# Kernel tuning notes

Measured on AMD Instinct MI355X. Metric: run time of the kernel, lower is better.

The kernel has to match this reference:

```python
import jax, jax.numpy as jnp
import numpy as np

EPS = float(np.finfo(np.float32).eps)


def setup_inputs() -> dict:
    key = jax.random.key(0)
    k1, k2, k3 = jax.random.split(key, 3)
    T, D, E = 8192, 2048, 64
    x = jax.random.normal(k1, (T, D), dtype=jnp.float32)
    wg_weight = jax.random.normal(k2, (E, D), dtype=jnp.float32) * 0.02
    u = jax.random.uniform(k3, (T, E), dtype=jnp.float32, minval=1e-6, maxval=1.0 - 1e-6)
    gumbel_noise = -jnp.log(-jnp.log(u))  # standard Gumbel(0,1) rsample
    return {"x": x, "wg_weight": wg_weight, "gumbel_noise": gumbel_noise}


def reference(x, wg_weight, gumbel_noise):
    # logits = wg(input): [T, E]
    logits = x @ wg_weight.T
    T, E = logits.shape
    capacity = 2 * ((T + E - 1) // E)  # training mode: 2 * ceil(T/E)

    gates = jax.nn.softmax(logits, axis=1)

    # top-1 expert
    idx1 = jnp.argmax(gates, axis=1)                       # [T]
    mask1 = jax.nn.one_hot(idx1, E, dtype=jnp.float32)     # [T, E]

    # second expert via gumbel-noised logits, masking out expert 1
    logits_w_noise = logits + gumbel_noise
    logits_except1 = jnp.where(mask1 > 0, -jnp.inf, logits_w_noise)
    idx2 = jnp.argmax(logits_except1, axis=1)
    mask2 = jax.nn.one_hot(idx2, E, dtype=jnp.float32)

    # capacity assignment: position of each token in its expert's queue
    locations1 = jnp.cumsum(mask1, axis=0) - 1.0           # [T, E]
    locations2 = jnp.cumsum(mask2, axis=0) - 1.0 + jnp.sum(mask1, axis=0, keepdims=True)

    # aux load-balancing loss
    me = jnp.mean(gates, axis=0)
    ce = jnp.mean(mask1, axis=0)
    l_aux = jnp.mean(me * ce) * E * E

    # drop tokens over capacity
    mask1 = mask1 * (locations1 < capacity)
    mask2 = mask2 * (locations2 < capacity)

    # gate values, renormalized over the two (kept) experts
    gates1_s = jnp.sum(gates * mask1, axis=1)
    gates2_s = jnp.sum(gates * mask2, axis=1)
    denom = jnp.maximum(gates1_s + gates2_s, EPS)
    gates1_s = gates1_s / denom
    gates2_s = gates2_s / denom

    # capacity slot index per token (0 for dropped tokens)
    loc1_s = jnp.sum(locations1 * mask1, axis=1).astype(jnp.int32)   # [T]
    loc2_s = jnp.sum(locations2 * mask2, axis=1).astype(jnp.int32)
    loc1_sc = jax.nn.one_hot(loc1_s, capacity, dtype=jnp.float32)    # [T, C]
    loc2_sc = jax.nn.one_hot(loc2_s, capacity, dtype=jnp.float32)

    # combine_weights[t, e, c] = gate_s[t] * mask[t, e] * onehot_loc[t, c]
    combine1 = jnp.einsum('t,te,tc->tec', gates1_s, mask1, loc1_sc)
    combine2 = jnp.einsum('t,te,tc->tec', gates2_s, mask2, loc2_sc)
    combine_weights = combine1 + combine2                   # [T, E, C]
    dispatch_mask = combine_weights.astype(bool)

    return l_aux, combine_weights, dispatch_mask
```

## Files before the change

kernel.cpp:

```cpp
#include <hip/hip_runtime.h>
#include <math.h>

#define T_TOK 8192
#define D_DIM 2048
#define E_EXP 64
#define CAP   256
#define NCHUNK 32
#define TEC   (134217728LL)
#define TE    (T_TOK * E_EXP)
#define KSPLIT 4
#define KLEN   (D_DIM / KSPLIT)

__device__ __forceinline__ int swz(int r) { return (r & 7) ^ ((r >> 3) & 7); }

__global__ __launch_bounds__(256) void k_gemm(const float* __restrict__ x,
                                              const float* __restrict__ wg,
                                              float* __restrict__ part) {
  __shared__ float xs[64 * 64];
  __shared__ float ws[64 * 64];
  const int tid = threadIdx.x;
  const int row0 = (blockIdx.x >> 2) * 64;
  const int kc = blockIdx.x & 3;
  const int kbase = kc * KLEN;
  const int tr = tid & 15;
  const int tc = tid >> 4;
  const int sA[4] = {swz(tr), swz(tr + 16), swz(tr + 32), swz(tr + 48)};
  const int sB[4] = {swz(tc * 4 + 0), swz(tc * 4 + 1), swz(tc * 4 + 2), swz(tc * 4 + 3)};
  float acc[4][4] = {{0.f, 0.f, 0.f, 0.f}, {0.f, 0.f, 0.f, 0.f},
                     {0.f, 0.f, 0.f, 0.f}, {0.f, 0.f, 0.f, 0.f}};
  for (int k0 = kbase; k0 < kbase + KLEN; k0 += 64) {
#pragma unroll
    for (int i = 0; i < 4; ++i) {
      const int f = tid + i * 256;
      const int r = f >> 4, g = f & 15;
      const float4 v = *reinterpret_cast<const float4*>(
          &x[(size_t)(row0 + r) * D_DIM + k0 + g * 4]);
      *reinterpret_cast<float4*>(&xs[r * 64 + ((g ^ swz(r)) << 2)]) = v;
    }
#pragma unroll
    for (int i = 0; i < 4; ++i) {
      const int f = tid + i * 256;
      const int r = f >> 4, g = f & 15;
      const float4 v = *reinterpret_cast<const float4*>(
          &wg[(size_t)r * D_DIM + k0 + g * 4]);
      *reinterpret_cast<float4*>(&ws[r * 64 + ((g ^ swz(r)) << 2)]) = v;
    }
    __syncthreads();
#pragma unroll
    for (int g = 0; g < 16; ++g) {
      float4 a[4], b[4];
#pragma unroll
      for (int j = 0; j < 4; ++j) {
        a[j] = *reinterpret_cast<const float4*>(&xs[(tr + 16 * j) * 64 + ((g ^ sA[j]) << 2)]);
        b[j] = *reinterpret_cast<const float4*>(&ws[(tc * 4 + j) * 64 + ((g ^ sB[j]) << 2)]);
      }
#pragma unroll
      for (int jr = 0; jr < 4; ++jr)
#pragma unroll
        for (int jc = 0; jc < 4; ++jc) {
          acc[jr][jc] = fmaf(a[jr].x, b[jc].x, acc[jr][jc]);
          acc[jr][jc] = fmaf(a[jr].y, b[jc].y, acc[jr][jc]);
          acc[jr][jc] = fmaf(a[jr].z, b[jc].z, acc[jr][jc]);
          acc[jr][jc] = fmaf(a[jr].w, b[jc].w, acc[jr][jc]);
        }
    }
    __syncthreads();
  }
  float* pbase = part + (size_t)kc * TE;
#pragma unroll
  for (int jr = 0; jr < 4; ++jr) {
    const float4 o = make_float4(acc[jr][0], acc[jr][1], acc[jr][2], acc[jr][3]);
    *reinterpret_cast<float4*>(&pbase[(size_t)(row0 + tr + 16 * jr) * E_EXP + tc * 4]) = o;
  }
}

__global__ __launch_bounds__(256) void k_gate(const float* __restrict__ part,
                                              const float* __restrict__ gumbel,
                                              float* __restrict__ colpart,
                                              int* __restrict__ idx1,
                                              int* __restrict__ idx2,
                                              float* __restrict__ g1v,
                                              float* __restrict__ g2v) {
  const int lane = threadIdx.x & 63;
  const int wave = threadIdx.x >> 6;
  const int gwave = blockIdx.x * 4 + wave;
  float colacc = 0.f;
  for (int i = 0; i < 4; ++i) {
    const int tA = gwave + i * 1024;
    const int tB = tA + 4096;
    const int oA = tA * 64 + lane;
    const int oB = tB * 64 + lane;
    const float LA = (part[oA] + part[TE + oA]) + (part[2 * TE + oA] + part[3 * TE + oA]);
    const float LB = (part[oB] + part[TE + oB]) + (part[2 * TE + oB] + part[3 * TE + oB]);
    const float gnA = gumbel[oA];
    const float gnB = gumbel[oB];
    float mA = LA; int iA = lane;
    float mB = LB; int iB = lane;
#pragma unroll
    for (int off = 32; off; off >>= 1) {
      const float vA = __shfl_xor(mA, off); const int jA = __shfl_xor(iA, off);
      const float vB = __shfl_xor(mB, off); const int jB = __shfl_xor(iB, off);
      if (vA > mA || (vA == mA && jA < iA)) { mA = vA; iA = jA; }
      if (vB > mB || (vB == mB && jB < iB)) { mB = vB; iB = jB; }
    }
    const float eA = expf(LA - mA);
    const float eB = expf(LB - mB);
    float sA = eA, sB = eB;
#pragma unroll
    for (int off = 32; off; off >>= 1) {
      sA += __shfl_xor(sA, off);
      sB += __shfl_xor(sB, off);
    }
    colacc += eA / sA + eB / sB;
    const float gate1A = 1.0f / sA;
    const float gate1B = 1.0f / sB;
    float nA = LA + gnA; if (lane == iA) nA = -INFINITY;
    float nB = LB + gnB; if (lane == iB) nB = -INFINITY;
    float vA2 = nA; int iA2 = lane;
    float vB2 = nB; int iB2 = lane;
#pragma unroll
    for (int off = 32; off; off >>= 1) {
      const float wA = __shfl_xor(vA2, off); const int kA = __shfl_xor(iA2, off);
      const float wB = __shfl_xor(vB2, off); const int kB = __shfl_xor(iB2, off);
      if (wA > vA2 || (wA == vA2 && kA < iA2)) { vA2 = wA; iA2 = kA; }
      if (wB > vB2 || (wB == vB2 && kB < iB2)) { vB2 = wB; iB2 = kB; }
    }
    const float gate2A = __shfl(eA, iA2) / sA;
    const float gate2B = __shfl(eB, iB2) / sB;
    if (lane == 0) {
      idx1[tA] = iA; idx2[tA] = iA2; g1v[tA] = gate1A; g2v[tA] = gate2A;
      idx1[tB] = iB; idx2[tB] = iB2; g1v[tB] = gate1B; g2v[tB] = gate2B;
    }
  }
  __shared__ float cs[4][64];
  cs[wave][lane] = colacc;
  __syncthreads();
  if (wave == 0) {
    float ssum = cs[0][lane] + cs[1][lane] + cs[2][lane] + cs[3][lane];
    colpart[blockIdx.x * 64 + lane] = ssum;
  }
}

__global__ __launch_bounds__(256) void k_rank(const int* __restrict__ idx1,
                                              const int* __restrict__ idx2,
                                              int* __restrict__ rank1,
                                              int* __restrict__ rank2,
                                              int* __restrict__ hist1,
                                              int* __restrict__ hist2) {
  __shared__ int s1[256], s2[256];
  __shared__ int h1[64], h2[64];
  const int tid = threadIdx.x;
  const int base = blockIdx.x * 256;
  if (tid < 64) { h1[tid] = 0; h2[tid] = 0; }
  s1[tid] = idx1[base + tid];
  s2[tid] = idx2[base + tid];
  __syncthreads();
  const int my1 = s1[tid], my2 = s2[tid];
  int r1 = 0, r2 = 0;
  for (int j = 0; j < 256; ++j) {
    r1 += (j < tid && s1[j] == my1);
    r2 += (j < tid && s2[j] == my2);
  }
  atomicAdd(&h1[my1], 1);
  atomicAdd(&h2[my2], 1);
  rank1[base + tid] = r1;
  rank2[base + tid] = r2;
  __syncthreads();
  if (tid < 64) {
    hist1[blockIdx.x * 64 + tid] = h1[tid];
    hist2[blockIdx.x * 64 + tid] = h2[tid];
  }
}

__global__ __launch_bounds__(256) void k_scatter(const int* __restrict__ idx1,
                                                 const int* __restrict__ idx2,
                                                 const float* __restrict__ g1v,
                                                 const float* __restrict__ g2v,
                                                 const int* __restrict__ rank1,
                                                 const int* __restrict__ rank2,
                                                 const int* __restrict__ hist1,
                                                 const int* __restrict__ hist2,
                                                 const float* __restrict__ colpart,
                                                 float* __restrict__ dout) {
  __shared__ int offs1_s[64], offs2_s[64];
  const int tid = threadIdx.x;
  const int bid = blockIdx.x;
  if (tid < 64) {
    const int e = tid;
    int run1 = 0, pre1 = 0;
    for (int c = 0; c < NCHUNK; ++c) {
      if (c == bid) pre1 = run1;
      run1 += hist1[c * 64 + e];
    }
    const int total1 = run1;
    int pre2 = 0;
    for (int c = 0; c < bid; ++c) pre2 += hist2[c * 64 + e];
    offs1_s[e] = pre1;
    offs2_s[e] = total1 + pre2;
    if (bid == 0) {
      float csum = 0.f;
      for (int b = 0; b < 256; ++b) csum += colpart[b * 64 + e];
      const float me = csum / (float)T_TOK;
      const float ce = (float)total1 / (float)T_TOK;
      float val = me * ce;
#pragma unroll
      for (int o = 32; o; o >>= 1) val += __shfl_xor(val, o);
      if (e == 0) dout[0] = val * (float)E_EXP;
    }
  }
  __syncthreads();
  const int t = bid * 256 + tid;
  const int e1 = idx1[t], e2 = idx2[t];
  const int loc1 = offs1_s[e1] + rank1[t];
  const int loc2 = offs2_s[e2] + rank2[t];
  const bool k1 = loc1 < CAP;
  const bool k2 = loc2 < CAP;
  const float a = k1 ? g1v[t] : 0.f;
  const float b = k2 ? g2v[t] : 0.f;
  const float denom = fmaxf(a + b, 1.1920929e-7f);
  if (k1) {
    const long long o = 1LL + ((long long)t * 64 + e1) * 256 + loc1;
    dout[o] = a / denom;
    dout[o + TEC] = 1.0f;
  }
  if (k2) {
    const long long o = 1LL + ((long long)t * 64 + e2) * 256 + loc2;
    dout[o] = b / denom;
    dout[o + TEC] = 1.0f;
  }
}

extern "C" void kernel_launch(void* const* d_in, const int* in_sizes, int n_in,
                              void* d_out, int out_size, void* d_ws, size_t ws_size,
                              hipStream_t stream) {
  const float* x = (const float*)d_in[0];
  const float* wg = (const float*)d_in[1];
  const float* gumbel = (const float*)d_in[2];
  float* dout = (float*)d_out;

  char* p = (char*)d_ws;
  float* part = (float*)p;              p += (size_t)KSPLIT * TE * 4;
  float* colpart = (float*)p;           p += 256 * 64 * 4;
  float* g1v = (float*)p;               p += T_TOK * 4;
  float* g2v = (float*)p;               p += T_TOK * 4;
  int* idx1 = (int*)p;                  p += T_TOK * 4;
  int* idx2 = (int*)p;                  p += T_TOK * 4;
  int* rank1 = (int*)p;                 p += T_TOK * 4;
  int* rank2 = (int*)p;                 p += T_TOK * 4;
  int* hist1 = (int*)p;                 p += NCHUNK * 64 * 4;
  int* hist2 = (int*)p;                 p += NCHUNK * 64 * 4;

  hipMemsetAsync(d_out, 0, (size_t)out_size * sizeof(float), stream);

  k_gemm<<<(T_TOK / 64) * KSPLIT, 256, 0, stream>>>(x, wg, part);
  k_gate<<<256, 256, 0, stream>>>(part, gumbel, colpart, idx1, idx2, g1v, g2v);
  k_rank<<<NCHUNK, 256, 0, stream>>>(idx1, idx2, rank1, rank2, hist1, hist2);
  k_scatter<<<NCHUNK, 256, 0, stream>>>(idx1, idx2, g1v, g2v, rank1, rank2,
                                        hist1, hist2, colpart, dout);
}
```

Baseline: 244.3 us.

## Fuse per-chunk ranking and histogram into gate kernel, drop rank kernel

```diff
diff --git a/kernel.cpp b/kernel.cpp
--- a/kernel.cpp
+++ b/kernel.cpp
@@ -5,7 +5,7 @@
 #define D_DIM 2048
 #define E_EXP 64
 #define CAP   256
-#define NCHUNK 32
+#define NCH   256
 #define TEC   (134217728LL)
 #define TE    (T_TOK * E_EXP)
 #define KSPLIT 4
@@ -80,14 +80,23 @@
                                               int* __restrict__ idx1,
                                               int* __restrict__ idx2,
                                               float* __restrict__ g1v,
-                                              float* __restrict__ g2v) {
-  const int lane = threadIdx.x & 63;
-  const int wave = threadIdx.x >> 6;
-  const int gwave = blockIdx.x * 4 + wave;
+                                              float* __restrict__ g2v,
+                                              int* __restrict__ rank1,
+                                              int* __restrict__ rank2,
+                                              int* __restrict__ hist1,
+                                              int* __restrict__ hist2) {
+  __shared__ int sIdx1[32], sIdx2[32];
+  __shared__ int h1[64], h2[64];
+  __shared__ float cs[4][64];
+  const int tid = threadIdx.x;
+  const int lane = tid & 63;
+  const int wave = tid >> 6;
+  const int base = blockIdx.x * 32;
+  if (tid < 64) { h1[tid] = 0; h2[tid] = 0; }
   float colacc = 0.f;
   for (int i = 0; i < 4; ++i) {
-    const int tA = gwave + i * 1024;
-    const int tB = tA + 4096;
+    const int tA = base + wave * 8 + i;
+    const int tB = tA + 4;
     const int oA = tA * 64 + lane;
     const int oB = tB * 64 + lane;
     const float LA = (part[oA] + part[TE + oA]) + (part[2 * TE + oA] + part[3 * TE + oA]);
@@ -128,43 +137,32 @@
     const float gate2A = __shfl(eA, iA2) / sA;
     const float gate2B = __shfl(eB, iB2) / sB;
     if (lane == 0) {
+      const int lt = wave * 8 + i;
+      sIdx1[lt] = iA; sIdx2[lt] = iA2;
+      sIdx1[lt + 4] = iB; sIdx2[lt + 4] = iB2;
       idx1[tA] = iA; idx2[tA] = iA2; g1v[tA] = gate1A; g2v[tA] = gate2A;
       idx1[tB] = iB; idx2[tB] = iB2; g1v[tB] = gate1B; g2v[tB] = gate2B;
     }
   }
-  __shared__ float cs[4][64];
   cs[wave][lane] = colacc;
   __syncthreads();
   if (wave == 0) {
-    float ssum = cs[0][lane] + cs[1][lane] + cs[2][lane] + cs[3][lane];
-    colpart[blockIdx.x * 64 + lane] = ssum;
-  }
-}
-
-__global__ __launch_bounds__(256) void k_rank(const int* __restrict__ idx1,
-                                              const int* __restrict__ idx2,
-                                              int* __restrict__ rank1,
-                                              int* __restrict__ rank2,
-                                              int* __restrict__ hist1,
-                                              int* __restrict__ hist2) {
-  __shared__ int s1[256], s2[256];
-  __shared__ int h1[64], h2[64];
-  const int tid = threadIdx.x;
-  const int base = blockIdx.x * 256;
-  if (tid < 64) { h1[tid] = 0; h2[tid] = 0; }
-  s1[tid] = idx1[base + tid];
-  s2[tid] = idx2[base + tid];
-  __syncthreads();
-  const int my1 = s1[tid], my2 = s2[tid];
-  int r1 = 0, r2 = 0;
-  for (int j = 0; j < 256; ++j) {
-    r1 += (j < tid && s1[j] == my1);
-    r2 += (j < tid && s2[j] == my2);
-  }
-  atomicAdd(&h1[my1], 1);
-  atomicAdd(&h2[my2], 1);
-  rank1[base + tid] = r1;
-  rank2[base + tid] = r2;
+    colpart[blockIdx.x * 64 + lane] =
+        (cs[0][lane] + cs[1][lane]) + (cs[2][lane] + cs[3][lane]);
+  }
+  if (tid < 32) {
+    const int my1 = sIdx1[tid], my2 = sIdx2[tid];
+    int r1 = 0, r2 = 0;
+#pragma unroll
+    for (int j = 0; j < 32; ++j) {
+      r1 += (j < tid && sIdx1[j] == my1);
+      r2 += (j < tid && sIdx2[j] == my2);
+    }
+    atomicAdd(&h1[my1], 1);
+    atomicAdd(&h2[my2], 1);
+    rank1[base + tid] = r1;
+    rank2[base + tid] = r2;
+  }
   __syncthreads();
   if (tid < 64) {
     hist1[blockIdx.x * 64 + tid] = h1[tid];
@@ -182,21 +180,22 @@
                                                  const int* __restrict__ hist2,
                                                  const float* __restrict__ colpart,
                                                  float* __restrict__ dout) {
-  __shared__ int offs1_s[64], offs2_s[64];
+  __shared__ int offs1_s[8][64], offs2_s[8][64];
   const int tid = threadIdx.x;
   const int bid = blockIdx.x;
   if (tid < 64) {
     const int e = tid;
-    int run1 = 0, pre1 = 0;
-    for (int c = 0; c < NCHUNK; ++c) {
-      if (c == bid) pre1 = run1;
+    int run1 = 0;
+    for (int c = 0; c < NCH; ++c) {
+      if ((c >> 3) == bid) offs1_s[c & 7][e] = run1;
       run1 += hist1[c * 64 + e];
     }
     const int total1 = run1;
-    int pre2 = 0;
-    for (int c = 0; c < bid; ++c) pre2 += hist2[c * 64 + e];
-    offs1_s[e] = pre1;
-    offs2_s[e] = total1 + pre2;
+    int run2 = 0;
+    for (int c = 0; c < NCH; ++c) {
+      if ((c >> 3) == bid) offs2_s[c & 7][e] = total1 + run2;
+      run2 += hist2[c * 64 + e];
+    }
     if (bid == 0) {
       float csum = 0.f;
       for (int b = 0; b < 256; ++b) csum += colpart[b * 64 + e];
@@ -210,9 +209,10 @@
   }
   __syncthreads();
   const int t = bid * 256 + tid;
+  const int cc = tid >> 5;
   const int e1 = idx1[t], e2 = idx2[t];
-  const int loc1 = offs1_s[e1] + rank1[t];
-  const int loc2 = offs2_s[e2] + rank2[t];
+  const int loc1 = offs1_s[cc][e1] + rank1[t];
+  const int loc2 = offs2_s[cc][e2] + rank2[t];
   const bool k1 = loc1 < CAP;
   const bool k2 = loc2 < CAP;
   const float a = k1 ? g1v[t] : 0.f;
@@ -247,14 +247,14 @@
   int* idx2 = (int*)p;                  p += T_TOK * 4;
   int* rank1 = (int*)p;                 p += T_TOK * 4;
   int* rank2 = (int*)p;                 p += T_TOK * 4;
-  int* hist1 = (int*)p;                 p += NCHUNK * 64 * 4;
-  int* hist2 = (int*)p;                 p += NCHUNK * 64 * 4;
+  int* hist1 = (int*)p;                 p += NCH * 64 * 4;
+  int* hist2 = (int*)p;                 p += NCH * 64 * 4;
 
   hipMemsetAsync(d_out, 0, (size_t)out_size * sizeof(float), stream);
 
   k_gemm<<<(T_TOK / 64) * KSPLIT, 256, 0, stream>>>(x, wg, part);
-  k_gate<<<256, 256, 0, stream>>>(part, gumbel, colpart, idx1, idx2, g1v, g2v);
-  k_rank<<<NCHUNK, 256, 0, stream>>>(idx1, idx2, rank1, rank2, hist1, hist2);
-  k_scatter<<<NCHUNK, 256, 0, stream>>>(idx1, idx2, g1v, g2v, rank1, rank2,
-                                        hist1, hist2, colpart, dout);
-}
+  k_gate<<<256, 256, 0, stream>>>(part, gumbel, colpart, idx1, idx2, g1v, g2v,
+                                  rank1, rank2, hist1, hist2);
+  k_scatter<<<NCH / 8, 256, 0, stream>>>(idx1, idx2, g1v, g2v, rank1, rank2,
+                                         hist1, hist2, colpart, dout);
+}
```

New measurement: 353.1 us. +44.5%, slower.
